# Optimization experiments

Measured on AMD Instinct MI355X. Metric: run time of the kernel, lower is better.

The kernel has to match this reference:

```python
import jax, jax.numpy as jnp
import numpy as np

CONF_THRES = 0.05  # DAGR.conf_threshold


def setup_inputs() -> dict:
    key = jax.random.key(0)
    B, N, C = 8, 100000, 80  # batch, candidate preds, num_classes
    # layout per row: [x, y, w, h, obj_conf, class_scores...]
    prediction = jax.random.uniform(key, (B, N, 5 + C), dtype=jnp.float32)
    return {"prediction": prediction}


def reference(prediction):
    """Batched, fixed-shape equivalent of postprocess_network_output's
    per-image conf-threshold filter + class argmax. Instead of ragged
    boolean filtering (data-dependent shapes), rows failing the confidence
    threshold are zeroed and a validity mask is returned.
    Returns:
      detections: [B, N, 7] = (x, y, w, h, obj_conf, class_conf, class_id)
      valid:      [B, N] bool mask (obj_conf >= conf_thres)
    """
    boxes = prediction[..., :4]                      # [B, N, 4]
    conf = prediction[..., 4]                        # [B, N]
    valid = conf >= CONF_THRES                       # [B, N] bool
    cls_scores = prediction[..., 5:]                 # [B, N, C]
    class_conf = jnp.max(cls_scores, axis=-1)        # [B, N]
    class_pred = jnp.argmax(cls_scores, axis=-1).astype(prediction.dtype)
    detections = jnp.concatenate(
        [boxes, conf[..., None], class_conf[..., None], class_pred[..., None]],
        axis=-1,
    )                                                # [B, N, 7]
    detections = detections * valid[..., None].astype(prediction.dtype)
    return detections, valid
```

## Files before the change

### kernel.cpp

```cpp
#include <hip/hip_runtime.h>


#define ROW      85
#define NCLS     80
#define TILE     64
#define THREADS  64
#define CONF_THRES 0.05f

__global__ __launch_bounds__(THREADS) void detect_kernel(
    const float* __restrict__ pred,
    float* __restrict__ det,
    float* __restrict__ valid,
    int rows)
{
    __shared__ float lds[TILE * ROW];
    __shared__ float lds_out[TILE * 7];

    const int tile0 = blockIdx.x * TILE;
    const int nrows = min(TILE, rows - tile0);
    if (nrows <= 0) return;

    if (nrows == TILE) {
        const float4* __restrict__ src = (const float4*)(pred + (size_t)tile0 * ROW);
        float4* dst = (float4*)lds;
        for (int i = threadIdx.x; i < (TILE * ROW) / 4; i += THREADS)
            dst[i] = src[i];
    } else {
        const float* __restrict__ src = pred + (size_t)tile0 * ROW;
        const int n = nrows * ROW;
        for (int i = threadIdx.x; i < n; i += THREADS)
            lds[i] = src[i];
    }
    __syncthreads();

    const int t = threadIdx.x;
    if (t < nrows) {
        const float* row = lds + t * ROW;
        const float x = row[0], y = row[1], w = row[2], h = row[3], conf = row[4];

        float best = row[5];
        int bidx = 0;
        #pragma unroll
        for (int k = 1; k < NCLS; ++k) {
            const float s = row[5 + k];
            if (s > best) { best = s; bidx = k; }
        }

        const float v = (conf >= CONF_THRES) ? 1.0f : 0.0f;
        float* o = lds_out + t * 7;
        o[0] = x * v;
        o[1] = y * v;
        o[2] = w * v;
        o[3] = h * v;
        o[4] = conf * v;
        o[5] = best * v;
        o[6] = (float)bidx * v;

        valid[tile0 + t] = v;
    }
    __syncthreads();

    if (nrows == TILE) {
        const float4* s4 = (const float4*)lds_out;
        float4* d4 = (float4*)(det + (size_t)tile0 * 7);
        for (int i = threadIdx.x; i < (TILE * 7) / 4; i += THREADS)
            d4[i] = s4[i];
    } else {
        float* d = det + (size_t)tile0 * 7;
        const int n = nrows * 7;
        for (int i = threadIdx.x; i < n; i += THREADS)
            d[i] = lds_out[i];
    }
}

extern "C" void kernel_launch(void* const* d_in, const int* in_sizes, int n_in,
                              void* d_out, int out_size, void* d_ws, size_t ws_size,
                              hipStream_t stream)
{
    const float* pred = (const float*)d_in[0];
    const int rows = in_sizes[0] / ROW;
    float* out = (float*)d_out;
    float* det = out;
    float* valid = out + (size_t)rows * 7;

    const int blocks = (rows + TILE - 1) / TILE;
    detect_kernel<<<blocks, THREADS, 0, stream>>>(pred, det, valid, rows);
}
```

Before: 416.0 us.

## Split class argmax across two half-waves and write detections directly to global

Doubles the block size to 128 threads so each row's 80-class argmax is split into two 40-class halves, merged with a cross-lane shuffle. The tile load is unrolled with a fixed trip count, and the output staging buffer in LDS plus its second barrier are removed, so lanes write their 7 outputs straight to global memory. This shortens the serial per-thread scan and raises parallelism per tile, at the cost of uncoalesced strided 7-float global stores. Rows past nrows in a partial tile now read uninitialised LDS, but those results are never stored.

```diff
diff --git a/kernel.cpp b/kernel.cpp
--- a/kernel.cpp
+++ b/kernel.cpp
@@ -4,7 +4,7 @@
 #define ROW      85
 #define NCLS     80
 #define TILE     64
-#define THREADS  64
+#define THREADS  128
 #define CONF_THRES 0.05f
 
 __global__ __launch_bounds__(THREADS) void detect_kernel(
@@ -14,7 +14,6 @@
     int rows)
 {
     __shared__ float lds[TILE * ROW];
-    __shared__ float lds_out[TILE * 7];
 
     const int tile0 = blockIdx.x * TILE;
     const int nrows = min(TILE, rows - tile0);
@@ -23,31 +22,42 @@
     if (nrows == TILE) {
         const float4* __restrict__ src = (const float4*)(pred + (size_t)tile0 * ROW);
         float4* dst = (float4*)lds;
-        for (int i = threadIdx.x; i < (TILE * ROW) / 4; i += THREADS)
-            dst[i] = src[i];
+        #pragma unroll
+        for (int it = 0; it < 10; ++it)
+            dst[threadIdx.x + THREADS * it] = src[threadIdx.x + THREADS * it];
+        if (threadIdx.x < 80)
+            dst[1280 + threadIdx.x] = src[1280 + threadIdx.x];
     } else {
         const float* __restrict__ src = pred + (size_t)tile0 * ROW;
-        const int n = nrows * ROW;
-        for (int i = threadIdx.x; i < n; i += THREADS)
+        for (int i = threadIdx.x; i < nrows * ROW; i += THREADS)
             lds[i] = src[i];
     }
     __syncthreads();
 
-    const int t = threadIdx.x;
-    if (t < nrows) {
-        const float* row = lds + t * ROW;
+    const int wave      = threadIdx.x >> 6;
+    const int lane      = threadIdx.x & 63;
+    const int half      = lane >> 5;
+    const int row_local = wave * 32 + (lane & 31);
+    const float* row    = lds + row_local * ROW;
+
+    const int kbase = half * 40;
+    float best = row[5 + kbase];
+    int   bidx = kbase;
+    #pragma unroll
+    for (int j = 1; j < 40; ++j) {
+        const float s = row[5 + kbase + j];
+        if (s > best) { best = s; bidx = kbase + j; }
+    }
+
+    const float obest = __shfl_xor(best, 32);
+    const int   oidx  = __shfl_xor(bidx, 32);
+    if (obest > best) { best = obest; bidx = oidx; }
+
+    if (half == 0 && row_local < nrows) {
         const float x = row[0], y = row[1], w = row[2], h = row[3], conf = row[4];
-
-        float best = row[5];
-        int bidx = 0;
-        #pragma unroll
-        for (int k = 1; k < NCLS; ++k) {
-            const float s = row[5 + k];
-            if (s > best) { best = s; bidx = k; }
-        }
-
         const float v = (conf >= CONF_THRES) ? 1.0f : 0.0f;
-        float* o = lds_out + t * 7;
+        const int   r = tile0 + row_local;
+        float* o = det + (size_t)r * 7;
         o[0] = x * v;
         o[1] = y * v;
         o[2] = w * v;
@@ -55,21 +65,7 @@
         o[4] = conf * v;
         o[5] = best * v;
         o[6] = (float)bidx * v;
-
-        valid[tile0 + t] = v;
-    }
-    __syncthreads();
-
-    if (nrows == TILE) {
-        const float4* s4 = (const float4*)lds_out;
-        float4* d4 = (float4*)(det + (size_t)tile0 * 7);
-        for (int i = threadIdx.x; i < (TILE * 7) / 4; i += THREADS)
-            d4[i] = s4[i];
-    } else {
-        float* d = det + (size_t)tile0 * 7;
-        const int n = nrows * 7;
-        for (int i = threadIdx.x; i < n; i += THREADS)
-            d[i] = lds_out[i];
+        valid[r] = v;
     }
 }
 
```

Result: faster. 363.4 us (-12.6%).
